# Kernel optimization log

Hardware: AMD Instinct MI355X
Metric: run time of the kernel (lower is better)

Reference implementation:

```python
import jax, jax.numpy as jnp
import numpy as np

INF = 100000000.0
TOPK = 27


def _box_iou(a, b):
    # a: [N,4] (x1,y1,x2,y2), b: [G,4] -> iou [N,G]
    area_a = (a[:, 2] - a[:, 0]) * (a[:, 3] - a[:, 1])
    area_b = (b[:, 2] - b[:, 0]) * (b[:, 3] - b[:, 1])
    lt = jnp.maximum(a[:, None, :2], b[None, :, :2])
    rb = jnp.minimum(a[:, None, 2:], b[None, :, 2:])
    wh = jnp.clip(rb - lt, 0.0)
    inter = wh[..., 0] * wh[..., 1]
    union = area_a[:, None] + area_b[None, :] - inter
    return inter / union, union


def _assign_one(anchors, gts, tokens):
    # anchors [N,4], gts [G,4], tokens [G,T]
    N = anchors.shape[0]
    G = gts.shape[0]
    ious, _ = _box_iou(anchors, gts)  # [N,G]

    a_cx = (anchors[:, 2] + anchors[:, 0]) * 0.5
    a_cy = (anchors[:, 3] + anchors[:, 1]) * 0.5
    g_cx = (gts[:, 2] + gts[:, 0]) * 0.5
    g_cy = (gts[:, 3] + gts[:, 1]) * 0.5

    # pairwise center distance [N,G]
    dist = jnp.sqrt((a_cx[:, None] - g_cx[None, :]) ** 2 +
                    (a_cy[:, None] - g_cy[None, :]) ** 2)

    # topk nearest anchors per gt (smallest distance) -> idxs [G,TOPK]
    _, topk_idxs = jax.lax.top_k(-dist.T, TOPK)

    # candidate ious [G,TOPK]
    cand = jnp.take_along_axis(ious.T, topk_idxs, axis=1)
    iou_mean = cand.mean(axis=1)
    iou_std = cand.std(axis=1, ddof=1)  # torch.std is unbiased
    is_pos = cand >= (iou_mean + iou_std)[:, None]

    # center-inside-gt check [G,TOPK]
    ax = a_cx[topk_idxs]
    ay = a_cy[topk_idxs]
    l = ax - gts[:, 0:1]
    t = ay - gts[:, 1:2]
    r = gts[:, 2:3] - ax
    b = gts[:, 3:4] - ay
    is_in_gts = jnp.minimum(jnp.minimum(l, t), jnp.minimum(r, b)) > 0.01
    is_pos = is_pos & is_in_gts

    # scatter candidate ious into flat [G*N] buffer of -INF (indices are unique)
    flat_idx = (jnp.arange(G)[:, None] * N + topk_idxs).reshape(-1)
    vals = ious.T.reshape(-1)[flat_idx]
    scat = jnp.where(is_pos.reshape(-1), vals, -INF)
    ious_inf = jnp.full((G * N,), -INF, dtype=ious.dtype).at[flat_idx].set(scat)
    ious_inf = ious_inf.reshape(G, N).T  # [N,G]

    anchors_to_gt_values = ious_inf.max(axis=1)          # [N]
    anchors_to_gt_indexs = ious_inf.argmax(axis=1)       # [N]

    matched_gts = gts[anchors_to_gt_indexs]              # [N,4]

    T = tokens.shape[1]
    unmatched = jnp.zeros((T,), tokens.dtype).at[-1].set(1.0)
    token_labels = jnp.where((anchors_to_gt_values == -INF)[:, None],
                             unmatched[None, :],
                             tokens[anchors_to_gt_indexs])  # [N,T]
    return anchors_to_gt_values, anchors_to_gt_indexs, matched_gts, token_labels


def setup_inputs() -> dict:
    key = jax.random.key(0)
    k1, k2, k3, k4, k5 = jax.random.split(key, 5)
    B, N, G, T = 8, 100000, 64, 256
    # anchors: valid x1<x2, y1<y2 boxes on a ~1024px canvas
    a_c = jax.random.uniform(k1, (B, N, 2), jnp.float32, 0.0, 1024.0)
    a_wh = jax.random.uniform(k2, (B, N, 2), jnp.float32, 8.0, 128.0)
    anchor_boxes = jnp.concatenate([a_c - a_wh / 2, a_c + a_wh / 2], axis=-1)
    g_c = jax.random.uniform(k3, (B, G, 2), jnp.float32, 0.0, 1024.0)
    g_wh = jax.random.uniform(k4, (B, G, 2), jnp.float32, 64.0, 512.0)
    gt_boxes = jnp.concatenate([g_c - g_wh / 2, g_c + g_wh / 2], axis=-1)
    token_map = jax.random.uniform(k5, (B, G, T), jnp.float32)
    return {"anchor_boxes": anchor_boxes, "gt_boxes": gt_boxes,
            "token_map": token_map}


def reference(anchor_boxes, gt_boxes, token_map):
    return jax.vmap(_assign_one)(anchor_boxes, gt_boxes, token_map)
```

## Files before the change

### kernel.cpp

```cpp
#include <hip/hip_runtime.h>
#include <cstdint>

constexpr int B = 8, N = 100000, G = 64, T = 256, TOPK = 27;
constexpr int BN = B * N;
constexpr int CAP = 1536;
constexpr int GPB = 2;
constexpr int WL_CAP = 16384;
constexpr int FILL_BLOCKS = 2048;
#define NEG_INF_VAL (-100000000.0f)

typedef float v4f __attribute__((ext_vector_type(4)));

__global__ __launch_bounds__(256) void atss_fillzero_kernel(
    unsigned long long* __restrict__ best, int* __restrict__ wl_cnt,
    float* __restrict__ out)
{
  const int t0 = blockIdx.x * 256 + threadIdx.x;
  const int NT = FILL_BLOCKS * 256;
  if (t0 == 0) *wl_cnt = 0;
  for (int i = t0; i < BN; i += NT) best[i] = 0ULL;

  v4f* __restrict__ tok = (v4f*)(out + (size_t)6 * BN);
  const int total = BN * (T / 4);
  for (int j = t0; j < total; j += NT) {
    v4f t = (v4f){0.0f, 0.0f, 0.0f, ((j & 63) == 63) ? 1.0f : 0.0f};
    tok[j] = t;
  }
}

__global__ __launch_bounds__(1024) void atss_assign_kernel(
    const float* __restrict__ anchors,
    const float* __restrict__ gts,
    unsigned long long* __restrict__ best,
    int* __restrict__ wl_cnt,
    int* __restrict__ worklist)
{
#pragma clang fp contract(off)
  __shared__ float s_d[GPB][CAP];
  __shared__ int   s_i[GPB][CAP];
  __shared__ int   s_cnt[GPB];
  __shared__ int   s_sel[GPB][TOPK];
  __shared__ float s_iou[GPB][TOPK];
  __shared__ int   s_in[GPB][TOPK];
  __shared__ float s_thresh;

  const int bid = blockIdx.x;
  const int p   = (bid & 7) * 32 + (bid >> 3);
  const int b   = p >> 5;
  const int g0  = (p & 31) * 2;
  const int bg0 = b * G + g0;
  const int tid = threadIdx.x;

  const float4 gb0 = ((const float4*)gts)[bg0];
  const float4 gb1 = ((const float4*)gts)[bg0 + 1];
  const float gcx0 = (gb0.z + gb0.x) * 0.5f, gcy0 = (gb0.w + gb0.y) * 0.5f;
  const float gcx1 = (gb1.z + gb1.x) * 0.5f, gcy1 = (gb1.w + gb1.y) * 0.5f;

  const float4* abase = (const float4*)(anchors + (size_t)b * N * 4);

  float thr2_0 = 576.0f, thr2_1 = 576.0f;
  int M0 = -1, M1 = -1;
  for (int attempt = 0; attempt < 8 && (M0 < 0 || M1 < 0); ++attempt) {
    if (tid == 0 && M0 < 0) s_cnt[0] = 0;
    if (tid == 1 && M1 < 0) s_cnt[1] = 0;
    __syncthreads();
    const bool a0 = (M0 < 0), a1 = (M1 < 0);

#define ATSS_TEST(ab, idx)                                                    \
  do {                                                                        \
    float cx = ((ab).z + (ab).x) * 0.5f;                                      \
    float cy = ((ab).w + (ab).y) * 0.5f;                                      \
    if (a0) {                                                                 \
      float dx = cx - gcx0, dy = cy - gcy0;                                   \
      float d2 = __fmul_rn(dx, dx) + __fmul_rn(dy, dy);                       \
      if (d2 < thr2_0) {                                                      \
        int q_ = atomicAdd(&s_cnt[0], 1);                                     \
        if (q_ < CAP) { s_d[0][q_] = __fsqrt_rn(d2); s_i[0][q_] = (idx); }    \
      }                                                                       \
    }                                                                         \
    if (a1) {                                                                 \
      float dx = cx - gcx1, dy = cy - gcy1;                                   \
      float d2 = __fmul_rn(dx, dx) + __fmul_rn(dy, dy);                       \
      if (d2 < thr2_1) {                                                      \
        int q_ = atomicAdd(&s_cnt[1], 1);                                     \
        if (q_ < CAP) { s_d[1][q_] = __fsqrt_rn(d2); s_i[1][q_] = (idx); }    \
      }                                                                       \
    }                                                                         \
  } while (0)

    for (int m = tid; m < N / 4; m += 1024) {
      float4 a0b = abase[4 * m];
      float4 a1b = abase[4 * m + 1];
      float4 a2b = abase[4 * m + 2];
      float4 a3b = abase[4 * m + 3];
      ATSS_TEST(a0b, 4 * m);
      ATSS_TEST(a1b, 4 * m + 1);
      ATSS_TEST(a2b, 4 * m + 2);
      ATSS_TEST(a3b, 4 * m + 3);
    }
#undef ATSS_TEST
    __syncthreads();
    const int c0 = s_cnt[0], c1 = s_cnt[1];
    __syncthreads();
    if (M0 < 0) {
      if (c0 >= TOPK && c0 <= CAP) M0 = c0;
      else thr2_0 *= (c0 < TOPK) ? 16.0f : 0.25f;
    }
    if (M1 < 0) {
      if (c1 >= TOPK && c1 <= CAP) M1 = c1;
      else thr2_1 *= (c1 < TOPK) ? 16.0f : 0.25f;
    }
  }

  for (int q = 0; q < GPB; ++q) {
    const int M = (q == 0) ? M0 : M1;
    const float4 gbox = (q == 0) ? gb0 : gb1;
    const int g = g0 + q;

    for (int s = tid; s < M; s += 1024) {
      unsigned long long pk_s =
          ((unsigned long long)__float_as_uint(s_d[q][s]) << 20) |
          (unsigned long long)(unsigned)s_i[q][s];
      int rank = 0;
      for (int j = 0; j < M; ++j) {
        unsigned long long pk_j =
            ((unsigned long long)__float_as_uint(s_d[q][j]) << 20) |
            (unsigned long long)(unsigned)s_i[q][j];
        rank += (pk_j < pk_s) ? 1 : 0;
      }
      if (rank < TOPK) s_sel[q][rank] = s_i[q][s];
    }
    __syncthreads();

    if (tid < TOPK) {
      int a = s_sel[q][tid];
      float4 ab = abase[a];
      float area_a = __fmul_rn(ab.z - ab.x, ab.w - ab.y);
      float area_b = __fmul_rn(gbox.z - gbox.x, gbox.w - gbox.y);
      float ltx = fmaxf(ab.x, gbox.x), lty = fmaxf(ab.y, gbox.y);
      float rbx = fminf(ab.z, gbox.z), rby = fminf(ab.w, gbox.w);
      float w = fmaxf(rbx - ltx, 0.0f), h = fmaxf(rby - lty, 0.0f);
      float inter = __fmul_rn(w, h);
      float uni = (area_a + area_b) - inter;
      s_iou[q][tid] = inter / uni;
      float acx = (ab.z + ab.x) * 0.5f, acy = (ab.w + ab.y) * 0.5f;
      float l = acx - gbox.x, t = acy - gbox.y;
      float r = gbox.z - acx, bt = gbox.w - acy;
      float mn = fminf(fminf(l, t), fminf(r, bt));
      s_in[q][tid] = (mn > 0.01f) ? 1 : 0;
    }
    __syncthreads();

    if (tid == 0) {
      float sum = 0.0f;
      for (int k = 0; k < TOPK; ++k) sum += s_iou[q][k];
      float mean = sum / (float)TOPK;
      float vs = 0.0f;
      for (int k = 0; k < TOPK; ++k) {
        float d = s_iou[q][k] - mean;
        vs += __fmul_rn(d, d);
      }
      float sd = __fsqrt_rn(vs / (float)(TOPK - 1));
      s_thresh = mean + sd;
    }
    __syncthreads();

    if (tid < TOPK) {
      float iou = s_iou[q][tid];
      bool pos = s_in[q][tid] && (iou >= s_thresh);
      if (pos) {
        unsigned long long pk =
            ((unsigned long long)__float_as_uint(iou) << 32) |
            (unsigned long long)(0xFFFFFFFFu - (unsigned)g);
        atomicMax(&best[(size_t)b * N + s_sel[q][tid]], pk);
      }
      unsigned long long mask = __ballot(pos);
      int nact = __popcll(mask);
      int base = 0;
      if (tid == 0 && nact > 0) base = atomicAdd(wl_cnt, nact);
      base = __shfl(base, 0);
      if (pos) {
        int rank = __popcll(mask & ((1ULL << tid) - 1ULL));
        worklist[base + rank] = b * N + s_sel[q][tid];
      }
    }
    __syncthreads();
  }
}

__global__ __launch_bounds__(256) void atss_scalar_write_kernel(
    const unsigned long long* __restrict__ best,
    const float* __restrict__ gts,
    float* __restrict__ out)
{
  float* __restrict__ out_val = out;
  float* __restrict__ out_idx = out + (size_t)BN;
  float* __restrict__ out_mg  = out + (size_t)2 * BN;

  const int i = blockIdx.x * 256 + threadIdx.x;
  unsigned long long p = best[i];
  const int b_ = i / N;
  int g = 0;
  float val = NEG_INF_VAL;
  if (p != 0ULL) {
    g   = (int)(0xFFFFFFFFu - (unsigned)(p & 0xFFFFFFFFULL));
    val = __uint_as_float((unsigned)(p >> 32));
  }
  const int row = b_ * G + g;
  out_val[i] = val;
  out_idx[i] = (float)g;
  ((v4f*)out_mg)[i] = ((const v4f*)gts)[row];
}

__global__ __launch_bounds__(256) void atss_token_scatter_kernel(
    const unsigned long long* __restrict__ best,
    const int* __restrict__ wl_cnt,
    const int* __restrict__ worklist,
    const float* __restrict__ tokens,
    float* __restrict__ out)
{
  const int w = blockIdx.x * 4 + (threadIdx.x >> 6);
  const int lane = threadIdx.x & 63;
  const int cnt = *wl_cnt;
  if (w >= cnt) return;
  const int i = worklist[w];
  const unsigned long long p = best[i];
  const int b_ = i / N;
  const int g  = (int)(0xFFFFFFFFu - (unsigned)(p & 0xFFFFFFFFULL));
  v4f t = ((const v4f*)tokens)[(size_t)(b_ * G + g) * 64 + lane];
  ((v4f*)(out + (size_t)6 * BN + (size_t)i * T))[lane] = t;
}

extern "C" void kernel_launch(void* const* d_in, const int* in_sizes, int n_in,
                              void* d_out, int out_size, void* d_ws, size_t ws_size,
                              hipStream_t stream) {
  const float* anchors = (const float*)d_in[0];
  const float* gts     = (const float*)d_in[1];
  const float* tokens  = (const float*)d_in[2];
  float* out = (float*)d_out;

  unsigned long long* best = (unsigned long long*)d_ws;
  int* wl_cnt   = (int*)((char*)d_ws + sizeof(unsigned long long) * (size_t)BN);
  int* worklist = wl_cnt + 16;

  atss_fillzero_kernel<<<FILL_BLOCKS, 256, 0, stream>>>(best, wl_cnt, out);
  atss_assign_kernel<<<B * G / GPB, 1024, 0, stream>>>(anchors, gts, best,
                                                       wl_cnt, worklist);
  atss_scalar_write_kernel<<<BN / 256, 256, 0, stream>>>(best, gts, out);
  atss_token_scatter_kernel<<<(WL_CAP + 1023) / 1024 * 256, 256, 0, stream>>>(
      best, wl_cnt, worklist, tokens, out);
}
```

Measured before the change: 862.7 us.

## Overlap token-buffer fill with assignment and merge the write kernels

The large default-token fill moves out of the zeroing kernel into extra blocks of the assignment kernel. The bandwidth-bound fill can then run alongside the latency-bound IoU/top-k work on otherwise idle CUs, and the zero kernel now only clears the packed best array. The scalar-output write and the token scatter are merged into one launch split by block index, which saves a kernel boundary. The cost is that fill blocks compete with assignment blocks for CUs and memory bandwidth, and the merged write kernel launches a fixed set of scatter blocks.

```diff
diff --git a/kernel.cpp b/kernel.cpp
--- a/kernel.cpp
+++ b/kernel.cpp
@@ -6,34 +6,29 @@
 constexpr int CAP = 1536;
 constexpr int GPB = 2;
 constexpr int WL_CAP = 16384;
-constexpr int FILL_BLOCKS = 2048;
+constexpr int ASSIGN_BLOCKS = B * G / GPB;
+constexpr int FAT_BLOCKS = 1024;
+constexpr int W1_BLOCKS = BN / 256;
+constexpr int SC_BLOCKS = WL_CAP / 4;
 #define NEG_INF_VAL (-100000000.0f)
 
 typedef float v4f __attribute__((ext_vector_type(4)));
 
-__global__ __launch_bounds__(256) void atss_fillzero_kernel(
-    unsigned long long* __restrict__ best, int* __restrict__ wl_cnt,
-    float* __restrict__ out)
+__global__ __launch_bounds__(256) void atss_zero_kernel(
+    unsigned long long* __restrict__ best, int* __restrict__ wl_cnt)
 {
   const int t0 = blockIdx.x * 256 + threadIdx.x;
-  const int NT = FILL_BLOCKS * 256;
   if (t0 == 0) *wl_cnt = 0;
-  for (int i = t0; i < BN; i += NT) best[i] = 0ULL;
-
-  v4f* __restrict__ tok = (v4f*)(out + (size_t)6 * BN);
-  const int total = BN * (T / 4);
-  for (int j = t0; j < total; j += NT) {
-    v4f t = (v4f){0.0f, 0.0f, 0.0f, ((j & 63) == 63) ? 1.0f : 0.0f};
-    tok[j] = t;
-  }
-}
-
-__global__ __launch_bounds__(1024) void atss_assign_kernel(
+  for (int i = t0; i < BN; i += 512 * 256) best[i] = 0ULL;
+}
+
+__global__ __launch_bounds__(1024) void atss_fat_kernel(
     const float* __restrict__ anchors,
     const float* __restrict__ gts,
     unsigned long long* __restrict__ best,
     int* __restrict__ wl_cnt,
-    int* __restrict__ worklist)
+    int* __restrict__ worklist,
+    float* __restrict__ out)
 {
 #pragma clang fp contract(off)
   __shared__ float s_d[GPB][CAP];
@@ -45,11 +40,24 @@
   __shared__ float s_thresh;
 
   const int bid = blockIdx.x;
+  const int tid = threadIdx.x;
+
+  if (bid >= ASSIGN_BLOCKS) {
+    const int fb  = bid - ASSIGN_BLOCKS;
+    const int NFT = (FAT_BLOCKS - ASSIGN_BLOCKS) * 1024;
+    v4f* __restrict__ tok = (v4f*)(out + (size_t)6 * BN);
+    const int total = BN * (T / 4);
+    for (int j = fb * 1024 + tid; j < total; j += NFT) {
+      v4f t = (v4f){0.0f, 0.0f, 0.0f, ((j & 63) == 63) ? 1.0f : 0.0f};
+      tok[j] = t;
+    }
+    return;
+  }
+
   const int p   = (bid & 7) * 32 + (bid >> 3);
   const int b   = p >> 5;
   const int g0  = (p & 31) * 2;
   const int bg0 = b * G + g0;
-  const int tid = threadIdx.x;
 
   const float4 gb0 = ((const float4*)gts)[bg0];
   const float4 gb1 = ((const float4*)gts)[bg0 + 1];
@@ -188,39 +196,40 @@
   }
 }
 
-__global__ __launch_bounds__(256) void atss_scalar_write_kernel(
+__global__ __launch_bounds__(256) void atss_write_kernel(
     const unsigned long long* __restrict__ best,
     const float* __restrict__ gts,
-    float* __restrict__ out)
-{
-  float* __restrict__ out_val = out;
-  float* __restrict__ out_idx = out + (size_t)BN;
-  float* __restrict__ out_mg  = out + (size_t)2 * BN;
-
-  const int i = blockIdx.x * 256 + threadIdx.x;
-  unsigned long long p = best[i];
-  const int b_ = i / N;
-  int g = 0;
-  float val = NEG_INF_VAL;
-  if (p != 0ULL) {
-    g   = (int)(0xFFFFFFFFu - (unsigned)(p & 0xFFFFFFFFULL));
-    val = __uint_as_float((unsigned)(p >> 32));
-  }
-  const int row = b_ * G + g;
-  out_val[i] = val;
-  out_idx[i] = (float)g;
-  ((v4f*)out_mg)[i] = ((const v4f*)gts)[row];
-}
-
-__global__ __launch_bounds__(256) void atss_token_scatter_kernel(
-    const unsigned long long* __restrict__ best,
     const int* __restrict__ wl_cnt,
     const int* __restrict__ worklist,
     const float* __restrict__ tokens,
     float* __restrict__ out)
 {
-  const int w = blockIdx.x * 4 + (threadIdx.x >> 6);
-  const int lane = threadIdx.x & 63;
+  const int bid = blockIdx.x;
+  const int tid = threadIdx.x;
+
+  if (bid < W1_BLOCKS) {
+    float* __restrict__ out_val = out;
+    float* __restrict__ out_idx = out + (size_t)BN;
+    float* __restrict__ out_mg  = out + (size_t)2 * BN;
+
+    const int i = bid * 256 + tid;
+    unsigned long long p = best[i];
+    const int b_ = i / N;
+    int g = 0;
+    float val = NEG_INF_VAL;
+    if (p != 0ULL) {
+      g   = (int)(0xFFFFFFFFu - (unsigned)(p & 0xFFFFFFFFULL));
+      val = __uint_as_float((unsigned)(p >> 32));
+    }
+    const int row = b_ * G + g;
+    out_val[i] = val;
+    out_idx[i] = (float)g;
+    ((v4f*)out_mg)[i] = ((const v4f*)gts)[row];
+    return;
+  }
+
+  const int w = (bid - W1_BLOCKS) * 4 + (tid >> 6);
+  const int lane = tid & 63;
   const int cnt = *wl_cnt;
   if (w >= cnt) return;
   const int i = worklist[w];
@@ -243,10 +252,9 @@
   int* wl_cnt   = (int*)((char*)d_ws + sizeof(unsigned long long) * (size_t)BN);
   int* worklist = wl_cnt + 16;
 
-  atss_fillzero_kernel<<<FILL_BLOCKS, 256, 0, stream>>>(best, wl_cnt, out);
-  atss_assign_kernel<<<B * G / GPB, 1024, 0, stream>>>(anchors, gts, best,
-                                                       wl_cnt, worklist);
-  atss_scalar_write_kernel<<<BN / 256, 256, 0, stream>>>(best, gts, out);
-  atss_token_scatter_kernel<<<(WL_CAP + 1023) / 1024 * 256, 256, 0, stream>>>(
-      best, wl_cnt, worklist, tokens, out);
-}
+  atss_zero_kernel<<<512, 256, 0, stream>>>(best, wl_cnt);
+  atss_fat_kernel<<<FAT_BLOCKS, 1024, 0, stream>>>(anchors, gts, best,
+                                                   wl_cnt, worklist, out);
+  atss_write_kernel<<<W1_BLOCKS + SC_BLOCKS, 256, 0, stream>>>(
+      best, gts, wl_cnt, worklist, tokens, out);
+}
```

Result: no change. 855.4 us (-0.9%).
